# Kernel tuning notes

Hardware: AMD Instinct MI355X
Metric: run time of the kernel (lower is better)

Reference implementation:

```python
import jax, jax.numpy as jnp
import numpy as np

EPS = 1e-5

def _conv3x3(x, w, stride=1):
    # x: [N,C,H,W], w: [O,C,3,3]
    return jax.lax.conv_general_dilated(
        x, w, window_strides=(stride, stride), padding=((1, 1), (1, 1)),
        dimension_numbers=('NCHW', 'OIHW', 'NCHW'))

def _bn(x, gamma, beta, mean, var):
    # eval-mode BatchNorm2d over channel axis 1
    inv = jax.lax.rsqrt(var + EPS)
    return (x - mean[None, :, None, None]) * (gamma * inv)[None, :, None, None] + beta[None, :, None, None]

def setup_inputs() -> dict:
    key = jax.random.key(0)
    ks = jax.random.split(key, 8)
    C = 128
    x = jax.random.normal(ks[0], (64, C, 56, 56), dtype=jnp.float32)
    w1 = jax.random.normal(ks[1], (C, C, 3, 3), dtype=jnp.float32) * 0.05
    w2 = jax.random.normal(ks[2], (C, C, 3, 3), dtype=jnp.float32) * 0.05
    gamma1 = jnp.ones((C,), jnp.float32)
    beta1 = jnp.zeros((C,), jnp.float32)
    mean1 = jax.random.normal(ks[3], (C,), dtype=jnp.float32) * 0.1
    var1 = jax.random.uniform(ks[4], (C,), minval=0.5, maxval=1.5, dtype=jnp.float32)
    gamma2 = jnp.ones((C,), jnp.float32)
    beta2 = jnp.zeros((C,), jnp.float32)
    mean2 = jax.random.normal(ks[5], (C,), dtype=jnp.float32) * 0.1
    var2 = jax.random.uniform(ks[6], (C,), minval=0.5, maxval=1.5, dtype=jnp.float32)
    return {"x": x, "w1": w1, "w2": w2,
            "gamma1": gamma1, "beta1": beta1, "mean1": mean1, "var1": var1,
            "gamma2": gamma2, "beta2": beta2, "mean2": mean2, "var2": var2}

def reference(x, w1, w2, gamma1, beta1, mean1, var1, gamma2, beta2, mean2, var2):
    # BasicBlock forward. The voting loop over global dict d is a no-op (d = {}).
    residual = x
    out = _conv3x3(x, w1, stride=1)
    out = jax.nn.relu(_bn(out, gamma1, beta1, mean1, var1))
    out = _conv3x3(out, w2, stride=1)
    out = _bn(out, gamma2, beta2, mean2, var2)
    return jax.nn.relu(out + residual)
```

## Files before the change

### kernel.cpp

```cpp
#include <hip/hip_runtime.h>
#include <cstdint>

typedef __attribute__((ext_vector_type(8))) short bf16x8;
typedef __attribute__((ext_vector_type(4))) float f32x4;
typedef unsigned short u16;
typedef uint32_t u32;

#define HW56 56
#define HWSQ 3136
#define MTOT 200704
#define CCH 128
#define BM 128
#define NSTEP 18

__device__ __forceinline__ u16 f2bf(float f) {
  u32 u = __builtin_bit_cast(u32, f);
  u = (u + 0x7fffu + ((u >> 16) & 1u)) >> 16;
  return (u16)u;
}
__device__ __forceinline__ float bf2f(u16 h) {
  return __builtin_bit_cast(float, (u32)h << 16);
}
__device__ __forceinline__ void gload16(const void* g, void* l) {
  __builtin_amdgcn_global_load_lds((const __attribute__((address_space(1))) void*)g,
                                   (__attribute__((address_space(3))) void*)l, 16, 0, 0);
}

__global__ __launch_bounds__(256) void pack_x_kernel(const float* __restrict__ x,
                                                     u16* __restrict__ xb) {
  const int lane = threadIdx.x & 63;
  const int wv = threadIdx.x >> 6;
  const int pos = blockIdx.x * 64 + lane;
  const int n = pos / HWSQ, hw = pos % HWSQ;
  const float* src = x + (size_t)n * (CCH * HWSQ) + hw;
  u16* dst = xb + (size_t)pos * CCH + wv * 32;
#pragma unroll
  for (int k = 0; k < 4; ++k) {
    u32 vv[4];
#pragma unroll
    for (int q = 0; q < 4; ++q) {
      const int c0 = wv * 32 + k * 8 + q * 2;
      u16 b0 = f2bf(src[(size_t)c0 * HWSQ]);
      u16 b1 = f2bf(src[(size_t)(c0 + 1) * HWSQ]);
      vv[q] = (u32)b0 | ((u32)b1 << 16);
    }
    uint4 v; v.x = vv[0]; v.y = vv[1]; v.z = vv[2]; v.w = vv[3];
    *(uint4*)(dst + k * 8) = v;
  }
}

__global__ __launch_bounds__(256) void pack_w_kernel(
    const float* __restrict__ w1, const float* __restrict__ w2,
    const float* __restrict__ g1, const float* __restrict__ be1,
    const float* __restrict__ mu1, const float* __restrict__ va1,
    const float* __restrict__ g2, const float* __restrict__ be2,
    const float* __restrict__ mu2, const float* __restrict__ va2,
    u16* __restrict__ w1p, u16* __restrict__ w2p,
    float* __restrict__ b1, float* __restrict__ b2, float* __restrict__ zp) {
  const int idx = blockIdx.x * 256 + threadIdx.x;
  if (idx < 2 * 147456) {
    const int which = idx >= 147456;
    const int j = which ? idx - 147456 : idx;
    const int t = j >> 14;
    const int oc = (j >> 7) & 127;
    const int ic = j & 127;
    const float* w = which ? w2 : w1;
    const float* gg = which ? g2 : g1;
    const float* va = which ? va2 : va1;
    const float s = gg[oc] * rsqrtf(va[oc] + 1e-5f);
    const float val = w[(size_t)(oc * 128 + ic) * 9 + t] * s;
    (which ? w2p : w1p)[j] = f2bf(val);
  }
  if (blockIdx.x == 0) {
    const int t = threadIdx.x;
    if (t < 128) {
      const float s1 = g1[t] * rsqrtf(va1[t] + 1e-5f);
      b1[t] = be1[t] - mu1[t] * s1;
      const float s2 = g2[t] * rsqrtf(va2[t] + 1e-5f);
      b2[t] = be2[t] - mu2[t] * s2;
    }
    if (t < 64) zp[t] = 0.f;
  }
}

template <int PASS>
__global__ __launch_bounds__(256, 2) void conv_mfma(
    const u16* __restrict__ src, const u16* __restrict__ wp,
    const float* __restrict__ bias, const u16* __restrict__ resid,
    u16* __restrict__ outb, float* __restrict__ outf,
    const char* __restrict__ zp) {
  __shared__ __align__(1024) char lds[65536];
  const int tid = threadIdx.x;
  const int wave = tid >> 6, lane = tid & 63;
  const int m0 = blockIdx.x * BM;
  const int wm = wave >> 1, wn = wave & 1;

  const int g = lane & 7;
  int ah[4], aw[4];
  long long aoff[4], boff[4];
#pragma unroll
  for (int i = 0; i < 4; ++i) {
    const int r = wave * 32 + i * 8 + (lane >> 3);
    const int pos = m0 + r;
    const int hw = pos % HWSQ;
    ah[i] = hw / HW56;
    aw[i] = hw % HW56;
    const int gsw = g ^ (r & 7);
    aoff[i] = (long long)pos * 256 + gsw * 16;
    boff[i] = (long long)r * 256 + gsw * 16;
  }
  const char* srcb = (const char*)src;
  const char* wpb = (const char*)wp;

  auto stage = [&](int buf, int s) {
    const int t = s >> 1, kh = s & 1;
    const int dyo = t / 3 - 1, dxo = t % 3 - 1;
    const long long adelta = (long long)(dyo * HW56 + dxo) * 256 + kh * 128;
    const long long bdelta = (long long)t * 32768 + kh * 128;
    char* ldsA = lds + buf * 16384;
    char* ldsB = lds + 32768 + buf * 16384;
#pragma unroll
    for (int i = 0; i < 4; ++i) {
      const int hh = ah[i] + dyo, ww = aw[i] + dxo;
      const bool valid = ((unsigned)hh < 56u) & ((unsigned)ww < 56u);
      const char* ap = valid ? (srcb + aoff[i] + adelta) : zp;
      gload16(ap, ldsA + (wave * 32 + i * 8) * 128);
      gload16(wpb + boff[i] + bdelta, ldsB + (wave * 32 + i * 8) * 128);
    }
  };

  f32x4 acc[4][4];
#pragma unroll
  for (int m = 0; m < 4; ++m)
#pragma unroll
    for (int n = 0; n < 4; ++n) {
      f32x4 z = {0.f, 0.f, 0.f, 0.f};
      acc[m][n] = z;
    }

  auto compute = [&](int buf) {
    const char* ldsA = lds + buf * 16384;
    const char* ldsB = lds + 32768 + buf * 16384;
    bf16x8 a[4][2], b[4][2];
#pragma unroll
    for (int m = 0; m < 4; ++m) {
      const int row = wm * 64 + m * 16 + (lane & 15);
      const char* rp = ldsA + row * 128;
      const int sw = row & 7;
#pragma unroll
      for (int ks = 0; ks < 2; ++ks) {
        const int gg = ks * 4 + (lane >> 4);
        a[m][ks] = *(const bf16x8*)(rp + ((gg ^ sw) << 4));
      }
    }
#pragma unroll
    for (int n = 0; n < 4; ++n) {
      const int row = wn * 64 + n * 16 + (lane & 15);
      const char* rp = ldsB + row * 128;
      const int sw = row & 7;
#pragma unroll
      for (int ks = 0; ks < 2; ++ks) {
        const int gg = ks * 4 + (lane >> 4);
        b[n][ks] = *(const bf16x8*)(rp + ((gg ^ sw) << 4));
      }
    }
#pragma unroll
    for (int ks = 0; ks < 2; ++ks)
#pragma unroll
      for (int m = 0; m < 4; ++m)
#pragma unroll
        for (int n = 0; n < 4; ++n)
          acc[m][n] = __builtin_amdgcn_mfma_f32_16x16x32_bf16(a[m][ks], b[n][ks],
                                                              acc[m][n], 0, 0, 0);
  };

  stage(0, 0);
  __syncthreads();
#pragma unroll
  for (int s = 0; s < NSTEP; ++s) {
    const int cur = s & 1;
    if (s + 1 < NSTEP) stage(cur ^ 1, s + 1);
    compute(cur);
    __syncthreads();
  }

  if (PASS == 1) {
#pragma unroll
    for (int nf = 0; nf < 4; ++nf) {
      const int oc = wn * 64 + nf * 16 + (lane & 15);
      const float bb = bias[oc];
#pragma unroll
      for (int m = 0; m < 4; ++m) {
        const int pbase = m0 + wm * 64 + m * 16 + (lane >> 4) * 4;
#pragma unroll
        for (int r = 0; r < 4; ++r) {
          float v = acc[m][nf][r] + bb;
          v = fmaxf(v, 0.f);
          outb[(size_t)(pbase + r) * CCH + oc] = f2bf(v);
        }
      }
    }
  } else {
    float* tl = (float*)(lds + wave * 4352);
    const int posr = m0 + wm * 64 + lane;
    const int nimg = posr / HWSQ, hwr = posr % HWSQ;
#pragma unroll
    for (int nf = 0; nf < 4; ++nf) {
      const int oc = wn * 64 + nf * 16 + (lane & 15);
      const float bb = bias[oc];
#pragma unroll
      for (int m = 0; m < 4; ++m) {
#pragma unroll
        for (int r = 0; r < 4; ++r) {
          const int row = m * 16 + (lane >> 4) * 4 + r;
          const int pos = m0 + wm * 64 + row;
          const float rv = bf2f(resid[(size_t)pos * CCH + oc]);
          float v = acc[m][nf][r] + bb + rv;
          tl[row * 17 + (lane & 15)] = fmaxf(v, 0.f);
        }
      }
#pragma unroll
      for (int oci = 0; oci < 16; ++oci) {
        const float v = tl[lane * 17 + oci];
        const int oc2 = wn * 64 + nf * 16 + oci;
        outf[(size_t)(nimg * CCH + oc2) * HWSQ + hwr] = v;
      }
    }
  }
}

extern "C" void kernel_launch(void* const* d_in, const int* in_sizes, int n_in,
                              void* d_out, int out_size, void* d_ws, size_t ws_size,
                              hipStream_t stream) {
  const float* x = (const float*)d_in[0];
  const float* w1 = (const float*)d_in[1];
  const float* w2 = (const float*)d_in[2];
  const float* g1 = (const float*)d_in[3];
  const float* be1 = (const float*)d_in[4];
  const float* mu1 = (const float*)d_in[5];
  const float* va1 = (const float*)d_in[6];
  const float* g2 = (const float*)d_in[7];
  const float* be2 = (const float*)d_in[8];
  const float* mu2 = (const float*)d_in[9];
  const float* va2 = (const float*)d_in[10];

  char* ws = (char*)d_ws;
  u16* xb  = (u16*)(ws + 0);
  u16* o1b = (u16*)(ws + 51380224);
  u16* w1p = (u16*)(ws + 102760448);
  u16* w2p = (u16*)(ws + 103055360);
  float* b1 = (float*)(ws + 103350272);
  float* b2 = (float*)(ws + 103350784);
  float* zp = (float*)(ws + 103351296);

  pack_x_kernel<<<MTOT / 64, 256, 0, stream>>>(x, xb);
  pack_w_kernel<<<1152, 256, 0, stream>>>(w1, w2, g1, be1, mu1, va1,
                                          g2, be2, mu2, va2, w1p, w2p, b1, b2, zp);
  conv_mfma<1><<<MTOT / BM, 256, 0, stream>>>(xb, w1p, b1, nullptr, o1b, nullptr,
                                              (const char*)zp);
  conv_mfma<2><<<MTOT / BM, 256, 0, stream>>>(o1b, w2p, b2, xb, nullptr, (float*)d_out,
                                              (const char*)zp);
}
```

Baseline: 347.0 us.

## Transpose x through LDS for coalesced packing and swizzle conv blocks per XCD

The NCHW-to-NHWC bf16 pack now stages a 128x64 tile in padded shared memory, so each thread no longer does scattered strided reads and writes. Global writes become contiguous 16-byte stores across positions. The conv kernels also remap block IDs so that each XCD handles a contiguous range of output rows, which should improve L2 locality for the halo rows shared between neighbouring tiles. This adds LDS use and a barrier to the pack kernel.

```diff
diff --git a/kernel.cpp b/kernel.cpp
--- a/kernel.cpp
+++ b/kernel.cpp
@@ -12,6 +12,8 @@
 #define CCH 128
 #define BM 128
 #define NSTEP 18
+#define NBLK (MTOT / BM)
+#define NB_PER_XCD (NBLK / 8)
 
 __device__ __forceinline__ u16 f2bf(float f) {
   u32 u = __builtin_bit_cast(u32, f);
@@ -28,24 +30,32 @@
 
 __global__ __launch_bounds__(256) void pack_x_kernel(const float* __restrict__ x,
                                                      u16* __restrict__ xb) {
-  const int lane = threadIdx.x & 63;
-  const int wv = threadIdx.x >> 6;
-  const int pos = blockIdx.x * 64 + lane;
-  const int n = pos / HWSQ, hw = pos % HWSQ;
-  const float* src = x + (size_t)n * (CCH * HWSQ) + hw;
-  u16* dst = xb + (size_t)pos * CCH + wv * 32;
-#pragma unroll
-  for (int k = 0; k < 4; ++k) {
+  __shared__ u16 t[128 * 65];
+  const int tid = threadIdx.x;
+  const int lane = tid & 63, wv = tid >> 6;
+  const int p0 = blockIdx.x * 64;
+  const int n = p0 / HWSQ, hw0 = p0 % HWSQ;
+  const float* src = x + (size_t)(n * CCH) * HWSQ + hw0;
+#pragma unroll
+  for (int k = 0; k < 32; ++k) {
+    const int c = wv * 32 + k;
+    t[c * 65 + lane] = f2bf(src[(size_t)c * HWSQ + lane]);
+  }
+  __syncthreads();
+  u16* dst = xb + (size_t)p0 * CCH;
+#pragma unroll
+  for (int it = 0; it < 4; ++it) {
+    const int u = it * 256 + tid;
+    const int pos = u >> 4, ch0 = (u & 15) * 8;
     u32 vv[4];
 #pragma unroll
     for (int q = 0; q < 4; ++q) {
-      const int c0 = wv * 32 + k * 8 + q * 2;
-      u16 b0 = f2bf(src[(size_t)c0 * HWSQ]);
-      u16 b1 = f2bf(src[(size_t)(c0 + 1) * HWSQ]);
-      vv[q] = (u32)b0 | ((u32)b1 << 16);
+      const u16 a = t[(ch0 + 2 * q) * 65 + pos];
+      const u16 b = t[(ch0 + 2 * q + 1) * 65 + pos];
+      vv[q] = (u32)a | ((u32)b << 16);
     }
     uint4 v; v.x = vv[0]; v.y = vv[1]; v.z = vv[2]; v.w = vv[3];
-    *(uint4*)(dst + k * 8) = v;
+    *(uint4*)(dst + (size_t)pos * CCH + ch0) = v;
   }
 }
 
@@ -92,7 +102,9 @@
   __shared__ __align__(1024) char lds[65536];
   const int tid = threadIdx.x;
   const int wave = tid >> 6, lane = tid & 63;
-  const int m0 = blockIdx.x * BM;
+  const int bid = blockIdx.x;
+  const int swz = (bid & 7) * NB_PER_XCD + (bid >> 3);
+  const int m0 = swz * BM;
   const int wm = wave >> 1, wn = wave & 1;
 
   const int g = lane & 7;
@@ -256,8 +268,8 @@
   pack_x_kernel<<<MTOT / 64, 256, 0, stream>>>(x, xb);
   pack_w_kernel<<<1152, 256, 0, stream>>>(w1, w2, g1, be1, mu1, va1,
                                           g2, be2, mu2, va2, w1p, w2p, b1, b2, zp);
-  conv_mfma<1><<<MTOT / BM, 256, 0, stream>>>(xb, w1p, b1, nullptr, o1b, nullptr,
-                                              (const char*)zp);
-  conv_mfma<2><<<MTOT / BM, 256, 0, stream>>>(o1b, w2p, b2, xb, nullptr, (float*)d_out,
-                                              (const char*)zp);
-}
+  conv_mfma<1><<<NBLK, 256, 0, stream>>>(xb, w1p, b1, nullptr, o1b, nullptr,
+                                         (const char*)zp);
+  conv_mfma<2><<<NBLK, 256, 0, stream>>>(o1b, w2p, b2, xb, nullptr, (float*)d_out,
+                                         (const char*)zp);
+}
```

After: 335.9 us. 3.2% less time.
